# Performance work log

Measured on AMD Instinct MI355X. Metric: run time of the kernel, lower is better.

## Reference

```python
import jax, jax.numpy as jnp
import numpy as np

_IDENTITY = jnp.array([1, 0, 0, 0], dtype=jnp.float32)

G, T, P, B = 512, 128, 256, 512  # num_graphs, max_terms, n_params, batch


def setup_inputs() -> dict:
    key = jax.random.key(0)
    k0, k1, k2, k3, k4 = jax.random.split(key, 5)
    psi_const = jax.random.randint(k0, (G, T), 0, 2).astype(jnp.int32)
    psi_params = jax.random.randint(k1, (G, T, P), 0, 2).astype(jnp.float32)
    phi_const = jax.random.randint(k2, (G, T), 0, 2).astype(jnp.int32)
    phi_params = jax.random.randint(k3, (G, T, P), 0, 2).astype(jnp.float32)
    param_vals = jax.random.randint(k4, (B, P), 0, 2).astype(jnp.float32)
    return {
        "psi_const": psi_const,
        "psi_params": psi_params,
        "phi_const": phi_const,
        "phi_params": phi_params,
        "param_vals": param_vals,
    }


def reference(psi_const, psi_params, phi_const, phi_params, param_vals):
    # GF(2) matmul: contract bitmasks with binary parameter values, mod 2.
    # psi_params: (G,T,P), param_vals: (B,P) -> (B,G,T)
    psi = jnp.mod(psi_const[None].astype(jnp.float32)
                  + jnp.einsum("gtp,bp->bgt", psi_params, param_vals), 2.0)
    phi = jnp.mod(phi_const[None].astype(jnp.float32)
                  + jnp.einsum("gtp,bp->bgt", phi_params, param_vals), 2.0)
    # Elementwise parity product and mod-2 sum over terms -> (B,G)
    exponent = jnp.mod(psi * phi, 2.0)
    sum_exponents = jnp.mod(jnp.sum(exponent, axis=-1), 2.0)
    # Parity-to-sign: (-1)^e = 1 - 2e, embedded as exact scalar (B,G,4)
    summands_exact = (1.0 - 2.0 * sum_exponents)[..., None] * _IDENTITY
    return summands_exact
```

## Files before the change

### kernel.cpp

```cpp
#include <hip/hip_runtime.h>

typedef unsigned long long u64;

#define G 512
#define T 128
#define P 256
#define B 512

#define PV_OFF    0
#define PSI_OFF   16384
#define PHI_OFF   (PSI_OFF + (size_t)G * T * 4 * 8)
#define CODES_OFF (PHI_OFF + (size_t)G * T * 4 * 8)
#define WS_NEEDED (CODES_OFF + (size_t)G * T * 4)


#define PSI_W (G * T * P / 64)
#define PHI_W PSI_W
#define PV_W  (B * P / 64)
#define TOTW  (PSI_W + PHI_W + PV_W)
#define PACK2_BLOCKS (TOTW / 256)

__device__ __forceinline__ unsigned nzbit(unsigned u) {
    return (u | (0u - u)) >> 31;
}

__global__ __launch_bounds__(256) void pack_words_kernel(
    const int*   __restrict__ psi_const,
    const int*   __restrict__ phi_const,
    const float* __restrict__ psi_params,
    const float* __restrict__ phi_params,
    const float* __restrict__ pv,
    u64*         __restrict__ psi_ws,
    u64*         __restrict__ phi_ws,
    u64*         __restrict__ pv_ws,
    unsigned*    __restrict__ codes_ws)
{
    const int tid = blockIdx.x * 256 + threadIdx.x;

    if (tid < G * T) {
        unsigned pc = ((unsigned)psi_const[tid]) & 1u;
        unsigned qc = ((unsigned)phi_const[tid]) & 1u;
        codes_ws[tid] = pc | (qc << 1);
    }

    const float* s;
    u64*         d;
    if (tid < PSI_W) {
        s = psi_params + (size_t)tid * 64;
        d = psi_ws + tid;
    } else if (tid < PSI_W + PHI_W) {
        int w = tid - PSI_W;
        s = phi_params + (size_t)w * 64;
        d = phi_ws + w;
    } else {
        int w = tid - PSI_W - PHI_W;
        s = pv + (size_t)w * 64;
        d = pv_ws + w;
    }

    const uint4* sv = (const uint4*)s;
    uint4 f[16];
    #pragma unroll
    for (int i = 0; i < 16; ++i) f[i] = sv[i];
    __builtin_amdgcn_sched_barrier(0);

    unsigned lo = 0, hi = 0;
    #pragma unroll
    for (int i = 0; i < 8; ++i) {
        lo |= nzbit(f[i].x) << (4 * i + 0);
        lo |= nzbit(f[i].y) << (4 * i + 1);
        lo |= nzbit(f[i].z) << (4 * i + 2);
        lo |= nzbit(f[i].w) << (4 * i + 3);
    }
    #pragma unroll
    for (int i = 8; i < 16; ++i) {
        hi |= nzbit(f[i].x) << (4 * (i - 8) + 0);
        hi |= nzbit(f[i].y) << (4 * (i - 8) + 1);
        hi |= nzbit(f[i].z) << (4 * (i - 8) + 2);
        hi |= nzbit(f[i].w) << (4 * (i - 8) + 3);
    }
    *d = ((u64)hi << 32) | (u64)lo;
}

__global__ __launch_bounds__(512) void pi_trans_kernel(
    const u64*      __restrict__ psi_ws,
    const u64*      __restrict__ phi_ws,
    const unsigned* __restrict__ codes,
    const u64*      __restrict__ pv,
    float4*         __restrict__ out)
{
    const int g    = blockIdx.x;
    const int lane = threadIdx.x & 63;
    const int wv   = threadIdx.x >> 6;

    u64 ra[8], rb[8];
    {
        const ulonglong2* pA0 = (const ulonglong2*)(psi_ws + ((size_t)g * T + lane) * 4);
        const ulonglong2* pB0 = (const ulonglong2*)(phi_ws + ((size_t)g * T + lane) * 4);
        const ulonglong2* pA1 = (const ulonglong2*)(psi_ws + ((size_t)g * T + lane + 64) * 4);
        const ulonglong2* pB1 = (const ulonglong2*)(phi_ws + ((size_t)g * T + lane + 64) * 4);
        ulonglong2 x;
        x = pA0[0]; ra[0] = x.x; ra[1] = x.y;
        x = pA0[1]; ra[2] = x.x; ra[3] = x.y;
        x = pB0[0]; ra[4] = x.x; ra[5] = x.y;
        x = pB0[1]; ra[6] = x.x; ra[7] = x.y;
        x = pA1[0]; rb[0] = x.x; rb[1] = x.y;
        x = pA1[1]; rb[2] = x.x; rb[3] = x.y;
        x = pB1[0]; rb[4] = x.x; rb[5] = x.y;
        x = pB1[1]; rb[6] = x.x; rb[7] = x.y;
    }
    unsigned ca = codes[g * T + lane];
    unsigned cb = codes[g * T + lane + 64];
    unsigned pa = ca & 1u, qa = (ca >> 1) & 1u;
    unsigned pb = cb & 1u, qb = (cb >> 1) & 1u;

    #pragma unroll
    for (int grp = 0; grp < 2; ++grp) {
        int b0  = wv * 64 + grp * 32;
        int b0u = __builtin_amdgcn_readfirstlane(b0);
        const u64* vp = pv + (size_t)b0u * 4;

        unsigned acc = 0;
        #pragma unroll
        for (int i = 0; i < 32; ++i) {
            u64 v0 = vp[i * 4 + 0], v1 = vp[i * 4 + 1];
            u64 v2 = vp[i * 4 + 2], v3 = vp[i * 4 + 3];
            u64 m0 = (ra[0] & v0) ^ (ra[1] & v1) ^ (ra[2] & v2) ^ (ra[3] & v3);
            u64 m1 = (ra[4] & v0) ^ (ra[5] & v1) ^ (ra[6] & v2) ^ (ra[7] & v3);
            u64 m2 = (rb[0] & v0) ^ (rb[1] & v1) ^ (rb[2] & v2) ^ (rb[3] & v3);
            u64 m3 = (rb[4] & v0) ^ (rb[5] & v1) ^ (rb[6] & v2) ^ (rb[7] & v3);
            unsigned f0 = (unsigned)m0 ^ (unsigned)(m0 >> 32);
            unsigned f1 = (unsigned)m1 ^ (unsigned)(m1 >> 32);
            unsigned f2 = (unsigned)m2 ^ (unsigned)(m2 >> 32);
            unsigned f3 = (unsigned)m3 ^ (unsigned)(m3 >> 32);
            unsigned t01 = ((unsigned)__popc(f0) ^ pa) & ((unsigned)__popc(f1) ^ qa);
            unsigned t23 = ((unsigned)__popc(f2) ^ pb) & ((unsigned)__popc(f3) ^ qb);
            acc ^= ((t01 ^ t23) & 1u) << i;
        }

        unsigned red = acc;
        #pragma unroll
        for (int m = 1; m < 64; m <<= 1)
            red ^= __shfl_xor(red, m, 64);

        if (lane < 32) {
            int b = b0u + lane;
            float s = 1.0f - 2.0f * (float)((red >> lane) & 1u);
            out[(size_t)b * G + g] = make_float4(s, 0.0f, 0.0f, 0.0f);
        }
    }
}

struct __align__(16) U64x2 { u64 x, y; };

__global__ __launch_bounds__(256) void pack_pv_kernel(
    const float* __restrict__ pv, u64* __restrict__ out)
{
    int lane = threadIdx.x & 63;
    int wave = threadIdx.x >> 6;
    int row  = blockIdx.x * 4 + wave;
    const float4* src = (const float4*)(pv + (size_t)row * P);
    float4 f = src[lane];
    u64 w0 = __ballot(f.x != 0.0f);
    u64 w1 = __ballot(f.y != 0.0f);
    u64 w2 = __ballot(f.z != 0.0f);
    u64 w3 = __ballot(f.w != 0.0f);
    if (lane == 0) {
        out[row * 4 + 0] = w0;
        out[row * 4 + 1] = w1;
        out[row * 4 + 2] = w2;
        out[row * 4 + 3] = w3;
    }
}

__global__ __launch_bounds__(512) void pi_main_kernel(
    const int*   __restrict__ psi_const,
    const float* __restrict__ psi_params,
    const int*   __restrict__ phi_const,
    const float* __restrict__ phi_params,
    const u64*   __restrict__ pv,
    float4*      __restrict__ out)
{
    __shared__ __align__(16) u64 rows[T * 8];
    __shared__ unsigned code_sm[T];

    const int g    = blockIdx.x;
    const int tid  = threadIdx.x;
    const int lane = tid & 63;
    const int wave = tid >> 6;

    if (tid < T) {
        unsigned pc = ((unsigned)psi_const[g * T + tid]) & 1u;
        unsigned qc = ((unsigned)phi_const[g * T + tid]) & 1u;
        code_sm[tid] = pc | (qc << 1);
    }

    for (int i = 0; i < 32; ++i) {
        int r = wave * 32 + i;
        int t = r & (T - 1);
        const float* mat = (r < T) ? psi_params : phi_params;
        int off = (r < T) ? 0 : 4;
        const float4* src = (const float4*)(mat + ((size_t)g * T + t) * P);
        float4 f = src[lane];
        u64 w0 = __ballot(f.x != 0.0f);
        u64 w1 = __ballot(f.y != 0.0f);
        u64 w2 = __ballot(f.z != 0.0f);
        u64 w3 = __ballot(f.w != 0.0f);
        if (lane == 0) {
            U64x2* d = (U64x2*)&rows[t * 8 + off];
            U64x2 a; a.x = w0; a.y = w1;
            U64x2 c; c.x = w2; c.y = w3;
            d[0] = a;
            d[1] = c;
        }
    }
    __syncthreads();

    const int b = tid;
    const u64* v = pv + (size_t)b * 4;
    u64 v0 = v[0], v1 = v[1], v2 = v[2], v3 = v[3];

    unsigned e = 0;
    #pragma unroll 8
    for (int t = 0; t < T; ++t) {
        const U64x2* row = (const U64x2*)&rows[t * 8];
        U64x2 p0 = row[0], p1 = row[1], q0 = row[2], q1 = row[3];
        u64 ma = (p0.x & v0) ^ (p0.y & v1) ^ (p1.x & v2) ^ (p1.y & v3);
        u64 mb = (q0.x & v0) ^ (q0.y & v1) ^ (q1.x & v2) ^ (q1.y & v3);
        unsigned c = code_sm[t];
        e ^= (((unsigned)__popcll(ma) ^ c) & ((unsigned)__popcll(mb) ^ (c >> 1)));
    }
    e &= 1u;

    float s = 1.0f - 2.0f * (float)e;
    out[(size_t)b * G + g] = make_float4(s, 0.0f, 0.0f, 0.0f);
}

extern "C" void kernel_launch(void* const* d_in, const int* in_sizes, int n_in,
                              void* d_out, int out_size, void* d_ws, size_t ws_size,
                              hipStream_t stream) {
    const int*   psi_const  = (const int*)  d_in[0];
    const float* psi_params = (const float*)d_in[1];
    const int*   phi_const  = (const int*)  d_in[2];
    const float* phi_params = (const float*)d_in[3];
    const float* param_vals = (const float*)d_in[4];

    if (ws_size >= WS_NEEDED) {
        u64*      pv_ws    = (u64*)((char*)d_ws + PV_OFF);
        u64*      psi_ws   = (u64*)((char*)d_ws + PSI_OFF);
        u64*      phi_ws   = (u64*)((char*)d_ws + PHI_OFF);
        unsigned* codes_ws = (unsigned*)((char*)d_ws + CODES_OFF);

        pack_words_kernel<<<PACK2_BLOCKS, 256, 0, stream>>>(
            psi_const, phi_const, psi_params, phi_params, param_vals,
            psi_ws, phi_ws, pv_ws, codes_ws);
        pi_trans_kernel<<<G, 512, 0, stream>>>(
            psi_ws, phi_ws, codes_ws, pv_ws, (float4*)d_out);
    } else {
        u64* pv_packed = (u64*)d_ws;
        pack_pv_kernel<<<B / 4, 256, 0, stream>>>(param_vals, pv_packed);
        pi_main_kernel<<<G, 512, 0, stream>>>(psi_const, psi_params,
                                              phi_const, phi_params,
                                              pv_packed, (float4*)d_out);
    }
}
```

Baseline: 191.4 us.

## Pack parameter bitmasks via global_load_lds staging and wave ballots

New measurement: 192.9 us. Within noise of the previous version (+0.8%).

```diff
diff --git a/kernel.cpp b/kernel.cpp
--- a/kernel.cpp
+++ b/kernel.cpp
@@ -1,6 +1,7 @@
 #include <hip/hip_runtime.h>
 
 typedef unsigned long long u64;
+typedef unsigned int u32;
 
 #define G 512
 #define T 128
@@ -10,82 +11,72 @@
 #define PV_OFF    0
 #define PSI_OFF   16384
 #define PHI_OFF   (PSI_OFF + (size_t)G * T * 4 * 8)
-#define CODES_OFF (PHI_OFF + (size_t)G * T * 4 * 8)
-#define WS_NEEDED (CODES_OFF + (size_t)G * T * 4)
-
-
-#define PSI_W (G * T * P / 64)
-#define PHI_W PSI_W
-#define PV_W  (B * P / 64)
-#define TOTW  (PSI_W + PHI_W + PV_W)
-#define PACK2_BLOCKS (TOTW / 256)
-
-__device__ __forceinline__ unsigned nzbit(unsigned u) {
-    return (u | (0u - u)) >> 31;
-}
-
-__global__ __launch_bounds__(256) void pack_words_kernel(
-    const int*   __restrict__ psi_const,
-    const int*   __restrict__ phi_const,
+#define WS_NEEDED (PHI_OFF + (size_t)G * T * 4 * 8)
+
+
+#define PSI_WORDS (G * T * 4)
+#define PV_WORDS  (B * 4)
+#define WPB       512
+#define CHUNKF    4096
+#define CHUNKS    (WPB * 64 / CHUNKF)
+#define PACK_BLOCKS ((2 * PSI_WORDS + PV_WORDS) / WPB)
+
+__global__ __launch_bounds__(256) void pack_dma_kernel(
     const float* __restrict__ psi_params,
     const float* __restrict__ phi_params,
     const float* __restrict__ pv,
-    u64*         __restrict__ psi_ws,
-    u64*         __restrict__ phi_ws,
-    u64*         __restrict__ pv_ws,
-    unsigned*    __restrict__ codes_ws)
-{
-    const int tid = blockIdx.x * 256 + threadIdx.x;
-
-    if (tid < G * T) {
-        unsigned pc = ((unsigned)psi_const[tid]) & 1u;
-        unsigned qc = ((unsigned)phi_const[tid]) & 1u;
-        codes_ws[tid] = pc | (qc << 1);
-    }
-
-    const float* s;
-    u64*         d;
-    if (tid < PSI_W) {
-        s = psi_params + (size_t)tid * 64;
-        d = psi_ws + tid;
-    } else if (tid < PSI_W + PHI_W) {
-        int w = tid - PSI_W;
-        s = phi_params + (size_t)w * 64;
-        d = phi_ws + w;
+    u64* __restrict__ psi_ws,
+    u64* __restrict__ phi_ws,
+    u64* __restrict__ pv_ws)
+{
+    __shared__ __align__(16) float stage[CHUNKF];
+
+    const int lane = threadIdx.x & 63;
+    const int wv   = threadIdx.x >> 6;
+    const int blk  = blockIdx.x;
+
+    const float* src;
+    u64*         dst;
+    if (blk < 512) {
+        src = psi_params + (size_t)blk * WPB * 64;
+        dst = psi_ws + (size_t)blk * WPB;
+    } else if (blk < 1024) {
+        src = phi_params + (size_t)(blk - 512) * WPB * 64;
+        dst = phi_ws + (size_t)(blk - 512) * WPB;
     } else {
-        int w = tid - PSI_W - PHI_W;
-        s = pv + (size_t)w * 64;
-        d = pv_ws + w;
-    }
-
-    const uint4* sv = (const uint4*)s;
-    uint4 f[16];
-    #pragma unroll
-    for (int i = 0; i < 16; ++i) f[i] = sv[i];
-    __builtin_amdgcn_sched_barrier(0);
-
-    unsigned lo = 0, hi = 0;
-    #pragma unroll
-    for (int i = 0; i < 8; ++i) {
-        lo |= nzbit(f[i].x) << (4 * i + 0);
-        lo |= nzbit(f[i].y) << (4 * i + 1);
-        lo |= nzbit(f[i].z) << (4 * i + 2);
-        lo |= nzbit(f[i].w) << (4 * i + 3);
-    }
-    #pragma unroll
-    for (int i = 8; i < 16; ++i) {
-        hi |= nzbit(f[i].x) << (4 * (i - 8) + 0);
-        hi |= nzbit(f[i].y) << (4 * (i - 8) + 1);
-        hi |= nzbit(f[i].z) << (4 * (i - 8) + 2);
-        hi |= nzbit(f[i].w) << (4 * (i - 8) + 3);
-    }
-    *d = ((u64)hi << 32) | (u64)lo;
+        src = pv + (size_t)(blk - 1024) * WPB * 64;
+        dst = pv_ws + (size_t)(blk - 1024) * WPB;
+    }
+
+    for (int c = 0; c < CHUNKS; ++c) {
+        const float* s0 = src + (size_t)c * CHUNKF + wv * 1024;
+        #pragma unroll
+        for (int k = 0; k < 4; ++k) {
+            __builtin_amdgcn_global_load_lds(
+                (const __attribute__((address_space(1))) u32*)(s0 + k * 256 + lane * 4),
+                (__attribute__((address_space(3))) u32*)&stage[wv * 1024 + k * 256],
+                16, 0, 0);
+        }
+        asm volatile("s_waitcnt vmcnt(0)" ::: "memory");
+        __syncthreads();
+
+        u64 myw = 0;
+        #pragma unroll
+        for (int r = 0; r < 16; ++r) {
+            float x = stage[r * 256 + wv * 64 + lane];
+            u64 bal = __ballot(x != 0.0f);
+            if (lane == r) myw = bal;
+        }
+        if (lane < 16) dst[c * 64 + lane * 4 + wv] = myw;
+        __syncthreads();
+    }
 }
 
 __global__ __launch_bounds__(512) void pi_trans_kernel(
+    const int*      __restrict__ psi_const,
+    const int*      __restrict__ phi_const,
     const u64*      __restrict__ psi_ws,
     const u64*      __restrict__ phi_ws,
-    const unsigned* __restrict__ codes,
     const u64*      __restrict__ pv,
     float4*         __restrict__ out)
 {
@@ -109,10 +100,10 @@
         x = pB1[0]; rb[4] = x.x; rb[5] = x.y;
         x = pB1[1]; rb[6] = x.x; rb[7] = x.y;
     }
-    unsigned ca = codes[g * T + lane];
-    unsigned cb = codes[g * T + lane + 64];
-    unsigned pa = ca & 1u, qa = (ca >> 1) & 1u;
-    unsigned pb = cb & 1u, qb = (cb >> 1) & 1u;
+    unsigned pa = ((unsigned)psi_const[g * T + lane]) & 1u;
+    unsigned qa = ((unsigned)phi_const[g * T + lane]) & 1u;
+    unsigned pb = ((unsigned)psi_const[g * T + lane + 64]) & 1u;
+    unsigned qb = ((unsigned)phi_const[g * T + lane + 64]) & 1u;
 
     #pragma unroll
     for (int grp = 0; grp < 2; ++grp) {
@@ -246,16 +237,14 @@
     const float* param_vals = (const float*)d_in[4];
 
     if (ws_size >= WS_NEEDED) {
-        u64*      pv_ws    = (u64*)((char*)d_ws + PV_OFF);
-        u64*      psi_ws   = (u64*)((char*)d_ws + PSI_OFF);
-        u64*      phi_ws   = (u64*)((char*)d_ws + PHI_OFF);
-        unsigned* codes_ws = (unsigned*)((char*)d_ws + CODES_OFF);
-
-        pack_words_kernel<<<PACK2_BLOCKS, 256, 0, stream>>>(
-            psi_const, phi_const, psi_params, phi_params, param_vals,
-            psi_ws, phi_ws, pv_ws, codes_ws);
+        u64* pv_ws  = (u64*)((char*)d_ws + PV_OFF);
+        u64* psi_ws = (u64*)((char*)d_ws + PSI_OFF);
+        u64* phi_ws = (u64*)((char*)d_ws + PHI_OFF);
+
+        pack_dma_kernel<<<PACK_BLOCKS, 256, 0, stream>>>(
+            psi_params, phi_params, param_vals, psi_ws, phi_ws, pv_ws);
         pi_trans_kernel<<<G, 512, 0, stream>>>(
-            psi_ws, phi_ws, codes_ws, pv_ws, (float4*)d_out);
+            psi_const, phi_const, psi_ws, phi_ws, pv_ws, (float4*)d_out);
     } else {
         u64* pv_packed = (u64*)d_ws;
         pack_pv_kernel<<<B / 4, 256, 0, stream>>>(param_vals, pv_packed);
```
